# Optimization experiments

Measured on AMD Instinct MI355X. Metric: run time of the kernel, lower is better.

The kernel has to match this reference:

```python
import jax, jax.numpy as jnp
import numpy as np

H, D, HID = 16, 128, 2048
B, S = 2, 2048
NUM_BLOCKS, BLOCK_SIZE = 32, 128


def _rope(x, cos, sin):
    # x: [T, H, D]; cos/sin: [T, D/2] (neox / rotate-half style)
    half = x.shape[-1] // 2
    x1, x2 = x[..., :half], x[..., half:]
    c = cos[:, None, :]
    s = sin[:, None, :]
    return jnp.concatenate([x1 * c - x2 * s, x2 * c + x1 * s], axis=-1)


def setup_inputs() -> dict:
    key = jax.random.key(0)
    ks = jax.random.split(key, 6)
    T = B * S
    hidden_states = jax.random.normal(ks[0], (T, HID), jnp.float32)
    wqkv = jax.random.normal(ks[1], (HID, 3 * HID), jnp.float32) * 0.02
    bqkv = jax.random.normal(ks[2], (3 * HID,), jnp.float32) * 0.02
    wo = jax.random.normal(ks[3], (HID, HID), jnp.float32) * 0.02
    # rotary tables, base 10000, dim = head_size
    inv_freq = 1.0 / (10000.0 ** (jnp.arange(0, D, 2, dtype=jnp.float32) / D))  # [D/2]
    pos = jnp.tile(jnp.arange(S, dtype=jnp.float32), B)  # positions per token [T]
    ang = pos[:, None] * inv_freq[None, :]  # [T, D/2]
    cos, sin = jnp.cos(ang), jnp.sin(ang)
    k_cache = jnp.zeros((NUM_BLOCKS, BLOCK_SIZE, H, D), jnp.float32)
    v_cache = jnp.zeros((NUM_BLOCKS, BLOCK_SIZE, H, D), jnp.float32)
    cu_seqlen_prefill = jnp.array([0, S, 2 * S], jnp.int32)
    slots = jnp.arange(T, dtype=jnp.int32)
    return {"hidden_states": hidden_states, "cos": cos, "sin": sin,
            "wqkv": wqkv, "bqkv": bqkv, "wo": wo,
            "k_cache": k_cache, "v_cache": v_cache,
            "cu_seqlen_prefill": cu_seqlen_prefill, "slots": slots, "max_s": S}


def reference(hidden_states, cos, sin, wqkv, bqkv, wo, k_cache, v_cache,
              cu_seqlen_prefill, slots, max_s):
    T = hidden_states.shape[0]
    # fused QKV projection (c_attn)
    qkv = hidden_states @ wqkv + bqkv  # [T, 3*H*D]
    q, k, v = jnp.split(qkv, [H * D, 2 * H * D], axis=1)
    q = q.reshape(T, H, D)
    k = k.reshape(T, H, D)
    v = v.reshape(T, H, D)
    # rotary embedding on q and k (in-place in torch; functional here)
    q = _rope(q, cos, sin)
    k = _rope(k, cos, sin)
    # reshape_and_cache: scatter post-rope k and v into paged KV cache by slot
    kc = k_cache.reshape(-1, H, D).at[slots].set(k).reshape(k_cache.shape)
    vc = v_cache.reshape(-1, H, D).at[slots].set(v).reshape(v_cache.shape)
    # prefill flash attention: varlen causal; equal-length sequences here
    b, s = T // max_s, max_s
    qb = q.reshape(b, s, H, D)
    kb = k.reshape(b, s, H, D)
    vb = v.reshape(b, s, H, D)
    scale = D ** -0.5
    scores = jnp.einsum('bqhd,bkhd->bhqk', qb, kb) * scale  # [B,H,S,S]
    causal = jnp.tril(jnp.ones((s, s), bool))
    scores = jnp.where(causal[None, None], scores, jnp.finfo(scores.dtype).min)
    probs = jax.nn.softmax(scores, axis=-1)
    attn = jnp.einsum('bhqk,bkhd->bqhd', probs, vb).reshape(T, H * D)
    out = attn @ wo  # c_proj, no bias
    return out, kc, vc
```

## Files before the change

### kernel.cpp

```cpp
#include <hip/hip_runtime.h>

using f32x4  = __attribute__((ext_vector_type(4))) float;
using frag16 = __attribute__((ext_vector_type(8))) short;
using s16x4  = __attribute__((ext_vector_type(4))) short;
using s16x8  = __attribute__((ext_vector_type(8))) short;
using u32x4  = __attribute__((ext_vector_type(4))) unsigned;

#define DI __device__ __forceinline__

constexpr int HID  = 2048;
constexpr int NH   = 16;
constexpr int HD   = 128;
constexpr int TT   = 4096;
constexpr int SEQ  = 2048;
constexpr int NQKV = 3 * HID;
constexpr float SCL = 0.08838834764831845f * 1.4426950408889634f;

DI short f2bf(float f) {
  unsigned u = __builtin_bit_cast(unsigned, f);
  unsigned r = (u + 0x7fffu + ((u >> 16) & 1u)) >> 16;
  return (short)r;
}
DI float bf2f(short s) {
  unsigned u = ((unsigned)(unsigned short)s) << 16;
  return __builtin_bit_cast(float, u);
}
DI unsigned cvtpk(float lo, float hi) {
  unsigned r;
  asm("v_cvt_pk_bf16_f32 %0, %1, %2" : "=v"(r) : "v"(lo), "v"(hi));
  return r;
}

struct alignas(8) S4h { short a, b, c, d; };

__global__ void conv_f32_bf16(const float* __restrict__ in, short* __restrict__ out) {
  int gid = blockIdx.x * 256 + threadIdx.x;
  const float4* in4 = (const float4*)in;
  float4 v = in4[gid];
  S4h o{f2bf(v.x), f2bf(v.y), f2bf(v.z), f2bf(v.w)};
  ((S4h*)out)[gid] = o;
}

__global__ void transpose_conv(const float* __restrict__ in, short* __restrict__ out,
                               int ldin, int R) {
  __shared__ float t[64][65];
  int tid = threadIdx.x;
  int bx = blockIdx.x, by = blockIdx.y;
#pragma unroll
  for (int i = 0; i < 4; i++) {
    int idx = i * 256 + tid;
    int r = idx >> 4, c4 = idx & 15;
    size_t gi = (size_t)(by * 64 + r) * ldin + bx * 64 + c4 * 4;
    float4 v = *(const float4*)(in + gi);
    t[r][c4 * 4] = v.x; t[r][c4 * 4 + 1] = v.y;
    t[r][c4 * 4 + 2] = v.z; t[r][c4 * 4 + 3] = v.w;
  }
  __syncthreads();
#pragma unroll
  for (int i = 0; i < 4; i++) {
    int idx = i * 256 + tid;
    int r = idx >> 4, c4 = idx & 15;
    s16x4 o;
#pragma unroll
    for (int j = 0; j < 4; j++) o[j] = f2bf(t[c4 * 4 + j][r]);
    *(s16x4*)(out + (size_t)(bx * 64 + r) * R + by * 64 + c4 * 4) = o;
  }
}

#define GLDS(src, dst)                                                     \
  __builtin_amdgcn_global_load_lds(                                        \
      (const __attribute__((address_space(1))) void*)(src),                \
      (__attribute__((address_space(3))) void*)(dst), 16, 0, 0)

template <int EPI>
__global__ __launch_bounds__(256, 2) void gemm_bt(
    const short* __restrict__ A, const short* __restrict__ Bt,
    const float* __restrict__ bias, float* __restrict__ Cout,
    const float* __restrict__ cs, const float* __restrict__ sn,
    const int* __restrict__ slots,
    short* __restrict__ Qb, short* __restrict__ Kb, short* __restrict__ Vt,
    float* __restrict__ kc, float* __restrict__ vc,
    int M, int N, int K) {
  __shared__ alignas(16) short Al[128 * 64];
  __shared__ alignas(16) short Bl[128 * 64];
  const int tid = threadIdx.x;
  const int wid = tid >> 6, lane = tid & 63;
  const int wr = wid >> 1, wc = wid & 1;
  const int l15 = lane & 15, lg = lane >> 4;
  const int gx = gridDim.x;
  const int id = blockIdx.y * gx + blockIdx.x;
  const int nwg = gx * gridDim.y;
  const int swz = (id & 7) * (nwg >> 3) + (id >> 3);
  const int row0 = (swz / gx) * 128, col0 = (swz % gx) * 128;
  const int lr8 = lane >> 3, l7 = lane & 7;

  f32x4 acc[4][4];
#pragma unroll
  for (int i = 0; i < 4; i++)
#pragma unroll
    for (int j = 0; j < 4; j++) acc[i][j] = {0.f, 0.f, 0.f, 0.f};

  for (int kt = 0; kt < K; kt += 64) {
#pragma unroll
    for (int c = 0; c < 4; c++) {
      int chunk = c * 4 + wid;
      int r = chunk * 8 + lr8;
      int ke = (l7 * 8) ^ ((r & 7) * 8);
      GLDS(A + (size_t)(row0 + r) * K + kt + ke, Al + chunk * 512);
      GLDS(Bt + (size_t)(col0 + r) * K + kt + ke, Bl + chunk * 512);
    }
    __syncthreads();
#pragma unroll
    for (int kk = 0; kk < 2; kk++) {
      frag16 af[4], bfv[4];
#pragma unroll
      for (int ai = 0; ai < 4; ai++) {
        int r = wr * 64 + ai * 16 + l15;
        int k0 = kk * 32 + lg * 8;
        af[ai] = *(const frag16*)(Al + r * 64 + (k0 ^ ((r & 7) * 8)));
      }
#pragma unroll
      for (int bj = 0; bj < 4; bj++) {
        int r = wc * 16 + (bj & 1) * 32 + ((bj >> 1) << 6) + l15;
        int k0 = kk * 32 + lg * 8;
        bfv[bj] = *(const frag16*)(Bl + r * 64 + (k0 ^ ((r & 7) * 8)));
      }
#pragma unroll
      for (int ai = 0; ai < 4; ai++)
#pragma unroll
        for (int bj = 0; bj < 4; bj++)
          acc[ai][bj] = __builtin_amdgcn_mfma_f32_16x16x32_bf16(
              af[ai], bfv[bj], acc[ai][bj], 0, 0, 0);
    }
    __syncthreads();
  }

  if (EPI == 0) {
#pragma unroll
    for (int ai = 0; ai < 4; ai++) {
#pragma unroll
      for (int bj = 0; bj < 4; bj++) {
        int row = row0 + wr * 64 + ai * 16 + lg * 4;
        int col = col0 + wc * 16 + (bj & 1) * 32 + ((bj >> 1) << 6) + l15;
#pragma unroll
        for (int r = 0; r < 4; r++)
          Cout[(size_t)(row + r) * N + col] = acc[ai][bj][r];
      }
    }
  } else {
    const int sec = col0 >> 11;
    const int h = (col0 & 2047) >> 7;
#pragma unroll
    for (int ai = 0; ai < 4; ai++) {
#pragma unroll
      for (int bj = 0; bj < 2; bj++) {
        const int d1 = wc * 16 + bj * 32 + l15;
        const float b1 = bias[col0 + d1];
        const float b2 = bias[col0 + d1 + 64];
        const int base = h * 128 + d1;
#pragma unroll
        for (int r = 0; r < 4; r++) {
          const int tok = row0 + wr * 64 + ai * 16 + lg * 4 + r;
          float v1 = acc[ai][bj][r] + b1;
          float v2 = acc[ai][bj + 2][r] + b2;
          if (sec == 0) {
            float c = cs[tok * 64 + d1], s = sn[tok * 64 + d1];
            Qb[(size_t)tok * HID + base]      = f2bf((v1 * c - v2 * s) * SCL);
            Qb[(size_t)tok * HID + base + 64] = f2bf((v2 * c + v1 * s) * SCL);
          } else if (sec == 1) {
            float c = cs[tok * 64 + d1], s = sn[tok * 64 + d1];
            float o1 = v1 * c - v2 * s, o2 = v2 * c + v1 * s;
            int sl = slots[tok];
            Kb[(size_t)tok * HID + base]      = f2bf(o1);
            Kb[(size_t)tok * HID + base + 64] = f2bf(o2);
            kc[(size_t)sl * HID + base]      = o1;
            kc[(size_t)sl * HID + base + 64] = o2;
          } else {
            int sl = slots[tok];
            vc[(size_t)sl * HID + base]      = v1;
            vc[(size_t)sl * HID + base + 64] = v2;
            int tsub = tok & 63;
            int cp = (tok & ~63) + 16 * ((tsub >> 2) & 3) + 4 * (tsub & 3) + (tsub >> 4);
            Vt[(size_t)base * TT + cp]        = f2bf(v1);
            Vt[(size_t)(base + 64) * TT + cp] = f2bf(v2);
          }
        }
      }
    }
  }
}

__global__ __launch_bounds__(256, 2) void flash_attn5(
    const short* __restrict__ Qb, const short* __restrict__ Kb,
    const short* __restrict__ Vt, short* __restrict__ attn) {
  __shared__ alignas(16) short Klds[2][64 * 128];
  __shared__ alignas(16) short Vlds[2][128 * 64];
  __shared__ alignas(16) short plds[4][16 * 72];

  const int tid = threadIdx.x;
  const int w = tid >> 6, lane = tid & 63;
  const int l15 = lane & 15, lg = lane >> 4;
  const int bid = blockIdx.x;
  const int p = bid >> 5;
  const int bh = bid & 31;
  const int b = bh >> 4, h = bh & 15;
  short* pl = &plds[w][0];

  frag16 ones;
#pragma unroll
  for (int j = 0; j < 8; j++) ones[j] = (short)0x3F80;

  auto stage = [&](int kv0, int buf) {
#pragma unroll
    for (int ci = 0; ci < 4; ci++) {
      int cc = w * 4 + ci;
      int krow = cc * 4 + (lane >> 4);
      int kss = (lane & 15) ^ (krow & 15);
      GLDS(Kb + (size_t)(b * SEQ + kv0 + krow) * HID + h * HD + kss * 8,
           Klds[buf] + cc * 512);
      int vd = cc * 8 + (lane >> 3);
      int vss = (lane & 7) ^ (vd & 7);
      GLDS(Vt + (size_t)(h * HD + vd) * TT + b * SEQ + kv0 + vss * 8,
           Vlds[buf] + cc * 512);
    }
  };

  const int qrowH = (31 - p) * 64 + w * 16;
  const int qrowL = p * 64 + w * 16;
  const int ntH = 32 - p;

  frag16 qfH[4], qfL[4];
  {
    const short* qpH = Qb + (size_t)(b * SEQ + qrowH + l15) * HID + h * HD + lg * 8;
    const short* qpL = Qb + (size_t)(b * SEQ + qrowL + l15) * HID + h * HD + lg * 8;
#pragma unroll
    for (int ds = 0; ds < 4; ds++) {
      qfH[ds] = *(const frag16*)(qpH + ds * 32);
      qfL[ds] = *(const frag16*)(qpL + ds * 32);
    }
  }
  f32x4 oH[8], oL[8];
#pragma unroll
  for (int j = 0; j < 8; j++) { oH[j] = {0.f, 0.f, 0.f, 0.f}; oL[j] = {0.f, 0.f, 0.f, 0.f}; }
  f32x4 laH = {0.f, 0.f, 0.f, 0.f}, laL = {0.f, 0.f, 0.f, 0.f};
  float mrH = -1e30f, mrL = -1e30f;

  auto proc = [&](const frag16 (&qf)[4], f32x4 (&o)[8], f32x4& la, float& mr,
                  bool diag, const short* Kl, const short* Vl) {
    f32x4 sa[4];
#pragma unroll
    for (int f = 0; f < 4; f++) sa[f] = {0.f, 0.f, 0.f, 0.f};
    __builtin_amdgcn_s_setprio(1);
#pragma unroll
    for (int ds = 0; ds < 4; ds++) {
      int phys = (ds * 4 + lg) ^ l15;
#pragma unroll
      for (int f = 0; f < 4; f++) {
        frag16 kf = *(const frag16*)(Kl + (f * 16 + l15) * 128 + phys * 8);
        sa[f] = __builtin_amdgcn_mfma_f32_16x16x32_bf16(kf, qf[ds], sa[f], 0, 0, 0);
      }
    }
    __builtin_amdgcn_s_setprio(0);
    if (diag) {
      int ql = 16 * w + l15;
#pragma unroll
      for (int f = 0; f < 4; f++)
#pragma unroll
        for (int r = 0; r < 4; r++)
          if (f * 16 + lg * 4 + r > ql) sa[f][r] = -1e30f;
    }
    float pm = sa[0][0];
#pragma unroll
    for (int f = 0; f < 4; f++)
#pragma unroll
      for (int r = 0; r < 4; r++) pm = fmaxf(pm, sa[f][r]);
    pm = fmaxf(pm, __shfl_xor(pm, 16));
    pm = fmaxf(pm, __shfl_xor(pm, 32));
    if (__any(pm > mr + 8.f)) {
      float mn = fmaxf(mr, pm);
      float frl = exp2f(mr - mn);
      mr = mn;
      float fr4[4];
#pragma unroll
      for (int r = 0; r < 4; r++)
        fr4[r] = __shfl(frl, lg * 16 + lg * 4 + r);
#pragma unroll
      for (int r = 0; r < 4; r++) {
        la[r] *= fr4[r];
#pragma unroll
        for (int j = 0; j < 8; j++) o[j][r] *= fr4[r];
      }
    }
    float pe[4][4];
#pragma unroll
    for (int f = 0; f < 4; f++)
#pragma unroll
      for (int r = 0; r < 4; r++) pe[f][r] = exp2f(sa[f][r] - mr);
    unsigned wv[8];
#pragma unroll
    for (int r = 0; r < 4; r++) {
      wv[2 * r]     = cvtpk(pe[0][r], pe[1][r]);
      wv[2 * r + 1] = cvtpk(pe[2][r], pe[3][r]);
    }
    {
      u32x4* pb = (u32x4*)(pl + l15 * 72 + lg * 16);
      pb[0] = {wv[0], wv[1], wv[2], wv[3]};
      pb[1] = {wv[4], wv[5], wv[6], wv[7]};
    }
    asm volatile("s_waitcnt lgkmcnt(0)" ::: "memory");
    frag16 pf0 = *(const frag16*)(pl + l15 * 72 + lg * 8);
    frag16 pf1 = *(const frag16*)(pl + l15 * 72 + 32 + lg * 8);
    __builtin_amdgcn_s_setprio(1);
    la = __builtin_amdgcn_mfma_f32_16x16x32_bf16(pf0, ones, la, 0, 0, 0);
    la = __builtin_amdgcn_mfma_f32_16x16x32_bf16(pf1, ones, la, 0, 0, 0);
#pragma unroll
    for (int j = 0; j < 8; j++) {
      int d = j * 16 + l15;
      int p0 = lg ^ (d & 7);
      int p1 = (4 + lg) ^ (d & 7);
      frag16 vf0 = *(const frag16*)(Vl + d * 64 + p0 * 8);
      frag16 vf1 = *(const frag16*)(Vl + d * 64 + p1 * 8);
      o[j] = __builtin_amdgcn_mfma_f32_16x16x32_bf16(pf0, vf0, o[j], 0, 0, 0);
      o[j] = __builtin_amdgcn_mfma_f32_16x16x32_bf16(pf1, vf1, o[j], 0, 0, 0);
    }
    __builtin_amdgcn_s_setprio(0);
  };

  stage(0, 0);
  __syncthreads();

  int cur = 0;
  for (int t = 0; t < ntH; t++) {
    if (t + 1 < ntH) stage((t + 1) * 64, cur ^ 1);
    const short* Kl = &Klds[cur][0];
    const short* Vl = &Vlds[cur][0];
    proc(qfH, oH, laH, mrH, t == ntH - 1, Kl, Vl);
    if (t <= p) proc(qfL, oL, laL, mrL, t == p, Kl, Vl);
    __syncthreads();
    cur ^= 1;
  }

  {
    float inv[4];
#pragma unroll
    for (int r = 0; r < 4; r++) inv[r] = 1.f / laH[r];
    short* op = attn + (size_t)(b * SEQ + qrowH + lg * 4) * HID + h * HD + l15;
#pragma unroll
    for (int j = 0; j < 8; j++)
#pragma unroll
      for (int r = 0; r < 4; r++)
        op[(size_t)r * HID + j * 16] = f2bf(oH[j][r] * inv[r]);
  }
  {
    float inv[4];
#pragma unroll
    for (int r = 0; r < 4; r++) inv[r] = 1.f / laL[r];
    short* op = attn + (size_t)(b * SEQ + qrowL + lg * 4) * HID + h * HD + l15;
#pragma unroll
    for (int j = 0; j < 8; j++)
#pragma unroll
      for (int r = 0; r < 4; r++)
        op[(size_t)r * HID + j * 16] = f2bf(oL[j][r] * inv[r]);
  }
}

extern "C" void kernel_launch(void* const* d_in, const int* in_sizes, int n_in,
                              void* d_out, int out_size, void* d_ws, size_t ws_size,
                              hipStream_t stream) {
  const float* hidden = (const float*)d_in[0];
  const float* cosb   = (const float*)d_in[1];
  const float* sinb   = (const float*)d_in[2];
  const float* wqkv   = (const float*)d_in[3];
  const float* bqkv   = (const float*)d_in[4];
  const float* wo     = (const float*)d_in[5];
  const int*   slots  = (const int*)d_in[9];

  float* out = (float*)d_out;
  float* kc  = out + (size_t)TT * HID;
  float* vc  = kc + (size_t)TT * HID;

  short* ws    = (short*)d_ws;
  short* Abf   = ws;
  short* Wqkvt = Abf + 8388608;
  short* Wot   = Wqkvt + 12582912;
  short* Qb    = Wot + 4194304;
  short* Kb    = Qb + 8388608;
  short* Vt    = Kb + 8388608;
  short* attnb = Abf;

  conv_f32_bf16<<<8192, 256, 0, stream>>>(hidden, Abf);
  transpose_conv<<<dim3(96, 32), 256, 0, stream>>>(wqkv, Wqkvt, NQKV, HID);
  transpose_conv<<<dim3(32, 32), 256, 0, stream>>>(wo, Wot, HID, HID);
  gemm_bt<1><<<dim3(48, 32), 256, 0, stream>>>(
      Abf, Wqkvt, bqkv, nullptr, cosb, sinb, slots, Qb, Kb, Vt, kc, vc,
      TT, NQKV, HID);
  flash_attn5<<<512, 256, 0, stream>>>(Qb, Kb, Vt, attnb);
  gemm_bt<0><<<dim3(16, 32), 256, 0, stream>>>(
      attnb, Wot, nullptr, out, nullptr, nullptr, nullptr,
      nullptr, nullptr, nullptr, nullptr, nullptr, TT, HID, HID);
}
```

Measured before the change: 295.3 us.

## Keep attention probabilities in registers and transpose V in a separate kernel

The flash attention kernel now packs the exponentiated scores directly into MFMA A-operand registers. This drops the per-wave LDS round trip and its lgkmcnt wait. To make that register layout line up, the key order inside each 64-token tile of V is permuted differently. The QKV GEMM epilogue now writes V row-major with coalesced stores, and a new transpose kernel builds the permuted V^T layout. Before, the epilogue did scattered strided transposed stores. The cost is one extra kernel launch and an extra read and write of V.

```diff
diff --git a/kernel.cpp b/kernel.cpp
--- a/kernel.cpp
+++ b/kernel.cpp
@@ -41,9 +41,12 @@
   ((S4h*)out)[gid] = o;
 }
 
-__global__ void transpose_conv(const float* __restrict__ in, short* __restrict__ out,
+template <bool IN_F32, bool PERM>
+__global__ void transpose_conv(const void* __restrict__ in_, short* __restrict__ out,
                                int ldin, int R) {
   __shared__ float t[64][65];
+  const float* inf = (const float*)in_;
+  const short* ins = (const short*)in_;
   int tid = threadIdx.x;
   int bx = blockIdx.x, by = blockIdx.y;
 #pragma unroll
@@ -51,9 +54,15 @@
     int idx = i * 256 + tid;
     int r = idx >> 4, c4 = idx & 15;
     size_t gi = (size_t)(by * 64 + r) * ldin + bx * 64 + c4 * 4;
-    float4 v = *(const float4*)(in + gi);
-    t[r][c4 * 4] = v.x; t[r][c4 * 4 + 1] = v.y;
-    t[r][c4 * 4 + 2] = v.z; t[r][c4 * 4 + 3] = v.w;
+    if (IN_F32) {
+      float4 v = *(const float4*)(inf + gi);
+      t[r][c4 * 4] = v.x; t[r][c4 * 4 + 1] = v.y;
+      t[r][c4 * 4 + 2] = v.z; t[r][c4 * 4 + 3] = v.w;
+    } else {
+      s16x4 v = *(const s16x4*)(ins + gi);
+#pragma unroll
+      for (int j = 0; j < 4; j++) t[r][c4 * 4 + j] = bf2f(v[j]);
+    }
   }
   __syncthreads();
 #pragma unroll
@@ -62,7 +71,12 @@
     int r = idx >> 4, c4 = idx & 15;
     s16x4 o;
 #pragma unroll
-    for (int j = 0; j < 4; j++) o[j] = f2bf(t[c4 * 4 + j][r]);
+    for (int j = 0; j < 4; j++) {
+      int c = c4 * 4 + j;
+      int cs = PERM ? ((c >> 5) * 32 + ((c >> 2) & 1) * 16 + ((c >> 3) & 3) * 4 + (c & 3))
+                    : c;
+      o[j] = f2bf(t[cs][r]);
+    }
     *(s16x4*)(out + (size_t)(bx * 64 + r) * R + by * 64 + c4 * 4) = o;
   }
 }
@@ -78,7 +92,7 @@
     const float* __restrict__ bias, float* __restrict__ Cout,
     const float* __restrict__ cs, const float* __restrict__ sn,
     const int* __restrict__ slots,
-    short* __restrict__ Qb, short* __restrict__ Kb, short* __restrict__ Vt,
+    short* __restrict__ Qb, short* __restrict__ Kb, short* __restrict__ Vrow,
     float* __restrict__ kc, float* __restrict__ vc,
     int M, int N, int K) {
   __shared__ alignas(16) short Al[128 * 64];
@@ -179,10 +193,8 @@
             int sl = slots[tok];
             vc[(size_t)sl * HID + base]      = v1;
             vc[(size_t)sl * HID + base + 64] = v2;
-            int tsub = tok & 63;
-            int cp = (tok & ~63) + 16 * ((tsub >> 2) & 3) + 4 * (tsub & 3) + (tsub >> 4);
-            Vt[(size_t)base * TT + cp]        = f2bf(v1);
-            Vt[(size_t)(base + 64) * TT + cp] = f2bf(v2);
+            Vrow[(size_t)tok * HID + base]      = f2bf(v1);
+            Vrow[(size_t)tok * HID + base + 64] = f2bf(v2);
           }
         }
       }
@@ -190,12 +202,11 @@
   }
 }
 
-__global__ __launch_bounds__(256, 2) void flash_attn5(
+__global__ __launch_bounds__(256, 2) void flash_attn6(
     const short* __restrict__ Qb, const short* __restrict__ Kb,
     const short* __restrict__ Vt, short* __restrict__ attn) {
   __shared__ alignas(16) short Klds[2][64 * 128];
   __shared__ alignas(16) short Vlds[2][128 * 64];
-  __shared__ alignas(16) short plds[4][16 * 72];
 
   const int tid = threadIdx.x;
   const int w = tid >> 6, lane = tid & 63;
@@ -204,7 +215,6 @@
   const int p = bid >> 5;
   const int bh = bid & 31;
   const int b = bh >> 4, h = bh & 15;
-  short* pl = &plds[w][0];
 
   frag16 ones;
 #pragma unroll
@@ -296,20 +306,13 @@
     for (int f = 0; f < 4; f++)
 #pragma unroll
       for (int r = 0; r < 4; r++) pe[f][r] = exp2f(sa[f][r] - mr);
-    unsigned wv[8];
-#pragma unroll
-    for (int r = 0; r < 4; r++) {
-      wv[2 * r]     = cvtpk(pe[0][r], pe[1][r]);
-      wv[2 * r + 1] = cvtpk(pe[2][r], pe[3][r]);
-    }
-    {
-      u32x4* pb = (u32x4*)(pl + l15 * 72 + lg * 16);
-      pb[0] = {wv[0], wv[1], wv[2], wv[3]};
-      pb[1] = {wv[4], wv[5], wv[6], wv[7]};
-    }
-    asm volatile("s_waitcnt lgkmcnt(0)" ::: "memory");
-    frag16 pf0 = *(const frag16*)(pl + l15 * 72 + lg * 8);
-    frag16 pf1 = *(const frag16*)(pl + l15 * 72 + 32 + lg * 8);
+    u32x4 w0, w1;
+    w0[0] = cvtpk(pe[0][0], pe[0][1]); w0[1] = cvtpk(pe[0][2], pe[0][3]);
+    w0[2] = cvtpk(pe[1][0], pe[1][1]); w0[3] = cvtpk(pe[1][2], pe[1][3]);
+    w1[0] = cvtpk(pe[2][0], pe[2][1]); w1[1] = cvtpk(pe[2][2], pe[2][3]);
+    w1[2] = cvtpk(pe[3][0], pe[3][1]); w1[3] = cvtpk(pe[3][2], pe[3][3]);
+    frag16 pf0 = __builtin_bit_cast(frag16, w0);
+    frag16 pf1 = __builtin_bit_cast(frag16, w1);
     __builtin_amdgcn_s_setprio(1);
     la = __builtin_amdgcn_mfma_f32_16x16x32_bf16(pf0, ones, la, 0, 0, 0);
     la = __builtin_amdgcn_mfma_f32_16x16x32_bf16(pf1, ones, la, 0, 0, 0);
@@ -385,16 +388,18 @@
   short* Wot   = Wqkvt + 12582912;
   short* Qb    = Wot + 4194304;
   short* Kb    = Qb + 8388608;
-  short* Vt    = Kb + 8388608;
+  short* Vrow  = Kb + 8388608;
+  short* Vt    = Vrow + 8388608;
   short* attnb = Abf;
 
   conv_f32_bf16<<<8192, 256, 0, stream>>>(hidden, Abf);
-  transpose_conv<<<dim3(96, 32), 256, 0, stream>>>(wqkv, Wqkvt, NQKV, HID);
-  transpose_conv<<<dim3(32, 32), 256, 0, stream>>>(wo, Wot, HID, HID);
+  transpose_conv<true, false><<<dim3(96, 32), 256, 0, stream>>>(wqkv, Wqkvt, NQKV, HID);
+  transpose_conv<true, false><<<dim3(32, 32), 256, 0, stream>>>(wo, Wot, HID, HID);
   gemm_bt<1><<<dim3(48, 32), 256, 0, stream>>>(
-      Abf, Wqkvt, bqkv, nullptr, cosb, sinb, slots, Qb, Kb, Vt, kc, vc,
+      Abf, Wqkvt, bqkv, nullptr, cosb, sinb, slots, Qb, Kb, Vrow, kc, vc,
       TT, NQKV, HID);
-  flash_attn5<<<512, 256, 0, stream>>>(Qb, Kb, Vt, attnb);
+  transpose_conv<false, true><<<dim3(32, 64), 256, 0, stream>>>(Vrow, Vt, HID, TT);
+  flash_attn6<<<512, 256, 0, stream>>>(Qb, Kb, Vt, attnb);
   gemm_bt<0><<<dim3(16, 32), 256, 0, stream>>>(
       attnb, Wot, nullptr, out, nullptr, nullptr, nullptr,
       nullptr, nullptr, nullptr, nullptr, nullptr, TT, HID, HID);
```

New measurement: 289.2 us, median of 2. 1.02x faster.
